# Kernel tuning notes

Measured on AMD Instinct MI355X. Metric: run time of the kernel, lower is better.

## Reference

```python
import jax, jax.numpy as jnp
import numpy as np

B, T, D, H = 512, 128, 256, 512  # batch, seq_len, input_dim, hidden_dim
L = T  # dense output size == seq_len


def setup_inputs() -> dict:
    key = jax.random.key(0)
    ks = jax.random.split(key, 12)
    s = 0.05
    return {
        "inputs": jax.random.normal(ks[0], (B, T, D), jnp.float32),
        "target_indices": jax.random.randint(ks[1], (B, T), 0, T),
        "enc_Wih": jax.random.normal(ks[2], (4 * H, D), jnp.float32) * s,
        "enc_Whh": jax.random.normal(ks[3], (4 * H, H), jnp.float32) * s,
        "enc_bih": jnp.zeros((4 * H,), jnp.float32),
        "enc_bhh": jnp.zeros((4 * H,), jnp.float32),
        "dec_Wih": jax.random.normal(ks[4], (4 * H, D), jnp.float32) * s,
        "dec_Whh": jax.random.normal(ks[5], (4 * H, H), jnp.float32) * s,
        "dec_bih": jnp.zeros((4 * H,), jnp.float32),
        "dec_bhh": jnp.zeros((4 * H,), jnp.float32),
        "Wd": jax.random.normal(ks[6], (L, H), jnp.float32) * s,
        "bd": jnp.zeros((L,), jnp.float32),
        "Wr": jax.random.normal(ks[7], (4, H), jnp.float32) * (2.0 / np.sqrt(H)),
        "br": jnp.zeros((4,), jnp.float32),
    }


def _lstm_cell(x, h, c, Wih, Whh, bih, bhh):
    gates = x @ Wih.T + h @ Whh.T + bih + bhh
    i, f, g, o = jnp.split(gates, 4, axis=-1)  # torch gate order i,f,g,o
    c = jax.nn.sigmoid(f) * c + jax.nn.sigmoid(i) * jnp.tanh(g)
    h = jax.nn.sigmoid(o) * jnp.tanh(c)
    return h, c


def reference(inputs, target_indices, enc_Wih, enc_Whh, enc_bih, enc_bhh,
              dec_Wih, dec_Whh, dec_bih, dec_bhh, Wd, bd, Wr, br):
    b, t, d = inputs.shape
    hdim = enc_Whh.shape[1]

    # Encoder LSTM over time (identical every step in the original -> compute once)
    def enc_step(carry, x_t):
        h, c = carry
        h, c = _lstm_cell(x_t, h, c, enc_Wih, enc_Whh, enc_bih, enc_bhh)
        return (h, c), h

    h0 = jnp.zeros((b, hdim), inputs.dtype)
    _, enc_hs = jax.lax.scan(enc_step, (h0, h0), inputs.transpose(1, 0, 2))
    enc = enc_hs.transpose(1, 0, 2)  # [B, T, H]

    batch_ar = jnp.arange(b)

    def dec_step(carry, idx_t):
        h, c, mask, x = carry
        h, c = _lstm_cell(x, h, c, dec_Wih, dec_Whh, dec_bih, dec_bhh)
        scores = jnp.einsum('bh,bth->bt', h, enc)
        attn = jax.nn.softmax(scores, axis=-1)
        ctx = jnp.einsum('bt,bth->bh', attn, enc)
        logits = ctx @ Wd.T + bd                       # [B, L]
        logits = jnp.where(mask > 0, -jnp.inf, logits)  # mask previously selected
        rot = ctx @ Wr.T + br                          # [B, 4]
        idx = jnp.clip(idx_t, 0, t - 1)
        mask = jnp.maximum(mask, jax.nn.one_hot(idx, mask.shape[1], dtype=mask.dtype))
        x_next = inputs[batch_ar, idx]
        return (h, c, mask, x_next), (logits, rot)

    mask0 = jnp.zeros((b, Wd.shape[0]), inputs.dtype)
    x0 = jnp.zeros((b, d), inputs.dtype)
    _, (all_logits, all_rot) = jax.lax.scan(
        dec_step, (h0, h0, mask0, x0), target_indices.T)
    return all_logits.transpose(1, 0, 2), all_rot.transpose(1, 0, 2)
```

## Files before the change

kernel.cpp:

```cpp
#include <hip/hip_runtime.h>
#include <hip/hip_bf16.h>
#include <hip/hip_fp16.h>
#include <math.h>

#define B_ 512
#define T_ 128
#define D_ 256
#define H_ 512
#define L_ 128

#define NEG_BIG (-1e30f)

typedef __hip_bfloat16 bf16;
typedef _Float16 f16x8 __attribute__((ext_vector_type(8)));
typedef float f32x4 __attribute__((ext_vector_type(4)));

__device__ __forceinline__ f32x4 mfma16(f16x8 a, f16x8 b, f32x4 c) {
  return __builtin_amdgcn_mfma_f32_16x16x32_f16(a, b, c, 0, 0, 0);
}

__device__ __forceinline__ float sigm(float x) { return 1.0f / (1.0f + expf(-x)); }

__device__ __forceinline__ float bf2f_bits(unsigned short u) {
  unsigned int i = ((unsigned int)u) << 16;
  float f; __builtin_memcpy(&f, &i, 4);
  return f;
}
__device__ __forceinline__ unsigned short f2bf_bits(float f) {
  unsigned int i; __builtin_memcpy(&i, &f, 4);
  unsigned int r = i + 0x7FFFu + ((i >> 16) & 1u);
  return (unsigned short)(r >> 16);
}

template <int F32>
__device__ __forceinline__ float ld1t(const void* base, size_t idx) {
  if (F32) return ((const float*)base)[idx];
  unsigned short u; __builtin_memcpy(&u, (const bf16*)base + idx, 2);
  return bf2f_bits(u);
}
template <int F32>
__device__ __forceinline__ void load8t(const void* base, size_t idx, float* d) {
  if (F32) {
    float4 x = *(const float4*)((const float*)base + idx);
    float4 y = *(const float4*)((const float*)base + idx + 4);
    d[0] = x.x; d[1] = x.y; d[2] = x.z; d[3] = x.w;
    d[4] = y.x; d[5] = y.y; d[6] = y.z; d[7] = y.w;
  } else {
    union { float4 f4; unsigned short u[8]; } q;
    q.f4 = *(const float4*)((const bf16*)base + idx);
#pragma unroll
    for (int i = 0; i < 8; ++i) d[i] = bf2f_bits(q.u[i]);
  }
}
template <int F32>
__device__ __forceinline__ void st1t(void* base, size_t idx, float v) {
  if (F32) ((float*)base)[idx] = v;
  else {
    unsigned short u = f2bf_bits(v);
    __builtin_memcpy((bf16*)base + idx, &u, 2);
  }
}

__global__ void probe_kernel(const void* x, int* flag) {
  __shared__ int cnt;
  if (threadIdx.x == 0) cnt = 0;
  __syncthreads();
  const unsigned short* u = (const unsigned short*)x;
  int wild = 0;
  for (int i = threadIdx.x; i < 16384; i += 256) {
    float v = bf2f_bits(u[2 * i]);
    float av = fabsf(v);
    if (!(av <= 1024.0f) || (v != 0.0f && av < 1e-20f)) wild++;
  }
  atomicAdd(&cnt, wild);
  __syncthreads();
  if (threadIdx.x == 0) flag[0] = (cnt > 512) ? 1 : 0;
}

__global__ void zero_kernel(float* __restrict__ p, int n4) {
  int i = blockIdx.x * blockDim.x + threadIdx.x;
  if (i < n4) ((float4*)p)[i] = make_float4(0.f, 0.f, 0.f, 0.f);
}

__global__ void first_sel_kernel(const int* __restrict__ tidx, int* __restrict__ fs) {
  __shared__ int row[L_];
  __shared__ int idxs[T_];
  int b = blockIdx.x;
  row[threadIdx.x] = 1 << 30;
  int v = tidx[b * T_ + threadIdx.x];
  idxs[threadIdx.x] = min(max(v, 0), T_ - 1);
  __syncthreads();
  if (threadIdx.x == 0) {
    for (int s = 0; s < T_; ++s) {
      int idx = idxs[s];
      if (row[idx] > s) row[idx] = s;
    }
  }
  __syncthreads();
  fs[b * L_ + threadIdx.x] = row[threadIdx.x];
}

template <int F32>
__device__ void pack_w_body(const void* Wih, const void* Whh, const void* bih,
                            const void* bhh, __half* Wpk, float* bs) {
  int np = blockIdx.x;
  int g = np & 3, j = np >> 2;
  int worig = g * H_ + j;
  for (int k = threadIdx.x; k < D_ + H_; k += 256) {
    float v = (k < D_) ? ld1t<F32>(Wih, (size_t)worig * D_ + k)
                       : ld1t<F32>(Whh, (size_t)worig * H_ + (k - D_));
    Wpk[(size_t)np * (D_ + H_) + k] = __float2half(v);
  }
  if (threadIdx.x == 0)
    bs[np] = ld1t<F32>(bih, worig) + ld1t<F32>(bhh, worig);
}
__global__ __launch_bounds__(256) void pack_w(const void* Wih, const void* Whh,
    const void* bih, const void* bhh, __half* Wpk, float* bs, const int* flagp) {
  if (*flagp) pack_w_body<1>(Wih, Whh, bih, bhh, Wpk, bs);
  else        pack_w_body<0>(Wih, Whh, bih, bhh, Wpk, bs);
}

template <int F32>
__device__ void pack16_body(const void* src, __half* dst, int n8) {
  int i = blockIdx.x * blockDim.x + threadIdx.x;
  if (i >= n8) return;
  float w[8];
  load8t<F32>(src, (size_t)i * 8, w);
  union { float4 f4; __half h[8]; } u;
#pragma unroll
  for (int q = 0; q < 8; ++q) u.h[q] = __float2half(w[q]);
  *(float4*)(dst + (size_t)i * 8) = u.f4;
}
__global__ __launch_bounds__(256) void pack16(const void* src, __half* dst, int n8,
                                              const int* flagp) {
  if (*flagp) pack16_body<1>(src, dst, n8);
  else        pack16_body<0>(src, dst, n8);
}

__global__ __launch_bounds__(256) void gather_x(const __half* __restrict__ X16,
                                                const int* __restrict__ tidx,
                                                __half* __restrict__ Xdec) {
  const int row = blockIdx.x * 8 + (threadIdx.x >> 5);
  const int c8 = (threadIdx.x & 31) * 8;
  const int b = row >> 7;
  const int s = row & (T_ - 1);
  float4 v;
  if (s == 0) {
    v = make_float4(0.f, 0.f, 0.f, 0.f);
  } else {
    int tsel = min(max(tidx[b * T_ + s - 1], 0), T_ - 1);
    v = *(const float4*)(X16 + ((size_t)b * T_ + tsel) * D_ + c8);
  }
  *(float4*)(Xdec + (size_t)row * D_ + c8) = v;
}

__global__ __launch_bounds__(256) void transpose_enc(const __half* __restrict__ enc,
                                                     __half* __restrict__ encT) {
  __shared__ __half tile[32][33];
  const int b = blockIdx.x;
  const int t0 = blockIdx.y * 32;
  const int h0 = blockIdx.z * 32;
  const int c = threadIdx.x & 31;
  const int r = threadIdx.x >> 5;
#pragma unroll
  for (int rr = 0; rr < 32; rr += 8)
    tile[rr + r][c] = enc[((size_t)b * T_ + t0 + rr + r) * H_ + h0 + c];
  __syncthreads();
#pragma unroll
  for (int rr = 0; rr < 32; rr += 8)
    encT[((size_t)b * H_ + h0 + rr + r) * T_ + t0 + c] = tile[c][rr + r];
}

#define SWZ(b, j) ((j) ^ (((b) & 7) << 2))

__device__ __forceinline__ void cell_f(const f32x4& acc, const float4& bias,
                                       float& c, float* hh) {
  float gi = acc[0] + bias.x;
  float gf = acc[1] + bias.y;
  float gg = acc[2] + bias.z;
  float go = acc[3] + bias.w;
  c = sigm(gf) * c + sigm(gi) * tanhf(gg);
  *hh = sigm(go) * tanhf(c);
}

template <int FAST>
__device__ void lstm_chain(const __half* __restrict__ Xp,
                           const __half* __restrict__ Wpk,
                           const float* __restrict__ bs,
                           __half* __restrict__ hbuf,
                           int tile, int bg, int* __restrict__ flags) {
  __shared__ __half hstage[32][32];
  const int tid = threadIdx.x;
  const int lane = tid & 63;
  const int w = tid >> 6;
  const int r15 = lane & 15;
  const int g4 = lane >> 4;
  const int m0 = tile * 128 + w * 32;
  const int b0 = bg * 32;
  const int bb0 = b0 + r15;
  const int bb1 = bb0 + 16;
  const int fl = lane & 15;
  const f32x4 z4 = {0.f, 0.f, 0.f, 0.f};

  const __half* aXp0 = Wpk + (size_t)(m0 + r15) * (D_ + H_) + g4 * 8;
  const __half* aXp1 = aXp0 + (size_t)16 * (D_ + H_);
  f16x8 aH0[16], aH1[16];
#pragma unroll
  for (int ks = 0; ks < 16; ++ks) {
    aH0[ks] = *(const f16x8*)(aXp0 + D_ + ks * 32);
    aH1[ks] = *(const f16x8*)(aXp1 + D_ + ks * 32);
  }
  const int nb0 = m0 + g4 * 4;
  const float4 bias0 = *(const float4*)(bs + nb0);
  const float4 bias1 = *(const float4*)(bs + nb0 + 16);
  const int jrel0 = w * 8 + g4;
  const int jrel1 = jrel0 + 4;
  float c00 = 0.f, c01 = 0.f, c10 = 0.f, c11 = 0.f;
  const int srow = tid >> 3;
  const int schk = tid & 7;
  const int sposl = SWZ(srow, schk * 4);
  unsigned long long* gdst = (unsigned long long*)hbuf;
  const size_t gcol = (size_t)tile * 32 + schk * 4;

  for (int t = 0; t < T_; ++t) {
    f32x4 acc00 = z4, acc01 = z4, acc10 = z4, acc11 = z4;
    {
      const __half* x0p = Xp + ((size_t)bb0 * T_ + t) * D_ + g4 * 8;
      const __half* x1p = Xp + ((size_t)bb1 * T_ + t) * D_ + g4 * 8;
#pragma unroll
      for (int ks = 0; ks < 8; ++ks) {
        f16x8 a0 = *(const f16x8*)(aXp0 + ks * 32);
        f16x8 a1 = *(const f16x8*)(aXp1 + ks * 32);
        f16x8 bx0 = *(const f16x8*)(x0p + ks * 32);
        f16x8 bx1 = *(const f16x8*)(x1p + ks * 32);
        acc00 = mfma16(a0, bx0, acc00);
        acc01 = mfma16(a0, bx1, acc01);
        acc10 = mfma16(a1, bx0, acc10);
        acc11 = mfma16(a1, bx1, acc11);
      }
    }
    if (t) {
      int v = __hip_atomic_load(flags + fl, __ATOMIC_RELAXED,
                                __HIP_MEMORY_SCOPE_AGENT);
      while (!__all(v >= t)) {
        __builtin_amdgcn_s_sleep(1);
        v = __hip_atomic_load(flags + fl, __ATOMIC_RELAXED,
                              __HIP_MEMORY_SCOPE_AGENT);
      }
      const __half* h0p = hbuf + ((size_t)bb0 * T_ + (t - 1)) * H_ + g4 * 8;
      const __half* h1p = hbuf + ((size_t)bb1 * T_ + (t - 1)) * H_ + g4 * 8;
      asm volatile("" : "+v"(h0p), "+v"(h1p));
#pragma unroll
      for (int ks = 0; ks < 16; ++ks) {
        f16x8 bh0 = *(const f16x8*)(h0p + ks * 32);
        f16x8 bh1 = *(const f16x8*)(h1p + ks * 32);
        acc00 = mfma16(aH0[ks], bh0, acc00);
        acc01 = mfma16(aH0[ks], bh1, acc01);
        acc10 = mfma16(aH1[ks], bh0, acc10);
        acc11 = mfma16(aH1[ks], bh1, acc11);
      }
    }
    float h00, h01, h10, h11;
    cell_f(acc00, bias0, c00, &h00);
    cell_f(acc01, bias0, c01, &h01);
    cell_f(acc10, bias1, c10, &h10);
    cell_f(acc11, bias1, c11, &h11);
    hstage[r15][SWZ(r15, jrel0)] = __float2half(h00);
    hstage[r15 + 16][SWZ(r15 + 16, jrel0)] = __float2half(h01);
    hstage[r15][SWZ(r15, jrel1)] = __float2half(h10);
    hstage[r15 + 16][SWZ(r15 + 16, jrel1)] = __float2half(h11);
    __syncthreads();
    {
      unsigned long long val =
          *(const unsigned long long*)&hstage[srow][sposl];
      size_t gi = ((((size_t)(b0 + srow) * T_ + t) * H_) + gcol) >> 2;
      if (FAST)
        gdst[gi] = val;
      else
        __hip_atomic_store(gdst + gi, val, __ATOMIC_RELAXED,
                           __HIP_MEMORY_SCOPE_AGENT);
    }
    if (t + 1 < T_) {
      __syncthreads();
      if (tid == 0)
        __hip_atomic_store(flags + tile, t + 1, __ATOMIC_RELAXED,
                           __HIP_MEMORY_SCOPE_AGENT);
    }
  }
}

__global__ __launch_bounds__(256, 2) void lstm_persist(
    const __half* __restrict__ Xenc, const __half* __restrict__ Xdec,
    const __half* __restrict__ WpkE, const float* __restrict__ bsE,
    const __half* __restrict__ WpkD, const float* __restrict__ bsD,
    __half* __restrict__ enc, __half* __restrict__ hdec, int* __restrict__ bar) {
  const int wgid = blockIdx.x;
  const int xcd = wgid & 7;
  const int tile = (wgid >> 3) & 15;
  const int q = wgid >> 7;
  const int g = q * 8 + xcd;
  const int p = g >> 4;
  const int bg = g & 15;
  int* flags = bar + g * 16;
  int* xcca = bar + 512 + g * 16;
  const int tid = threadIdx.x;
  const int lane = tid & 63;

  int xcc;
  asm volatile("s_getreg_b32 %0, hwreg(HW_REG_XCC_ID)" : "=s"(xcc));
  if (tid == 0)
    __hip_atomic_store(xcca + tile, xcc + 1, __ATOMIC_RELAXED,
                       __HIP_MEMORY_SCOPE_AGENT);
  int vv = __hip_atomic_load(xcca + (lane & 15), __ATOMIC_RELAXED,
                             __HIP_MEMORY_SCOPE_AGENT);
  while (!__all(vv != 0)) {
    __builtin_amdgcn_s_sleep(1);
    vv = __hip_atomic_load(xcca + (lane & 15), __ATOMIC_RELAXED,
                           __HIP_MEMORY_SCOPE_AGENT);
  }
  const int fast = __all(vv == (xcc + 1));

  if (p == 0) {
    if (fast) lstm_chain<1>(Xenc, WpkE, bsE, enc, tile, bg, flags);
    else      lstm_chain<0>(Xenc, WpkE, bsE, enc, tile, bg, flags);
  } else {
    if (fast) lstm_chain<1>(Xdec, WpkD, bsD, hdec, tile, bg, flags);
    else      lstm_chain<0>(Xdec, WpkD, bsD, hdec, tile, bg, flags);
  }
}

template <int F32>
__device__ void attend_body(const __half* __restrict__ hdec, const __half* __restrict__ enc,
                            const __half* __restrict__ encT, const __half* __restrict__ Wd16,
                            const void* __restrict__ bd, const void* __restrict__ Wr,
                            const void* __restrict__ br, const int* __restrict__ fs,
                            void* __restrict__ out) {
  __shared__ __align__(16) __half Plds[4][16 * 128];
  __shared__ __align__(16) __half Clds[4][16 * 128];
  const int b = blockIdx.x;
  const int sbase = blockIdx.y * 64;
  const int tid = threadIdx.x;
  const int lane = tid & 63;
  const int w = tid >> 6;
  const int r15 = lane & 15;
  const int g4 = lane >> 4;
  const int sw = sbase + w * 16;
  const __half* encb = enc + (size_t)b * T_ * H_;
  const f32x4 z4 = {0.f, 0.f, 0.f, 0.f};
  f32x4 sacc[8];
#pragma unroll
  for (int i = 0; i < 8; ++i) sacc[i] = z4;
  {
    const __half* hdp = hdec + ((size_t)b * T_ + (sw + r15)) * H_ + g4 * 8;
    for (int k0 = 0; k0 < H_; k0 += 32) {
      f16x8 bv = *(const f16x8*)(hdp + k0);
      const __half* ap = encb + (size_t)r15 * H_ + g4 * 8 + k0;
#pragma unroll
      for (int ms = 0; ms < 8; ++ms)
        sacc[ms] = mfma16(*(const f16x8*)(ap + (size_t)ms * 16 * H_), bv, sacc[ms]);
    }
  }
  float mx = -INFINITY;
#pragma unroll
  for (int ms = 0; ms < 8; ++ms)
#pragma unroll
    for (int q = 0; q < 4; ++q) mx = fmaxf(mx, sacc[ms][q]);
  mx = fmaxf(mx, __shfl_xor(mx, 16));
  mx = fmaxf(mx, __shfl_xor(mx, 32));
  float sum = 0.f;
  float pv[32];
#pragma unroll
  for (int ms = 0; ms < 8; ++ms)
#pragma unroll
    for (int q = 0; q < 4; ++q) {
      float e = expf(sacc[ms][q] - mx);
      pv[ms * 4 + q] = e;
      sum += e;
    }
  sum += __shfl_xor(sum, 16);
  sum += __shfl_xor(sum, 32);
  const float inv = 1.0f / sum;
  {
    char* pw = (char*)Plds[w];
    const int swz = (r15 & 7) << 4;
#pragma unroll
    for (int ms = 0; ms < 8; ++ms)
#pragma unroll
      for (int q = 0; q < 4; ++q) {
        int t = ms * 16 + g4 * 4 + q;
        *(__half*)(pw + r15 * 256 + ((t * 2) ^ swz)) = __float2half(pv[ms * 4 + q] * inv);
      }
  }
  __syncthreads();
  f32x4 lacc[8];
#pragma unroll
  for (int i = 0; i < 8; ++i) lacc[i] = z4;
  float racc = 0.f;
  const int sl4 = lane >> 2;
  const int rr4 = lane & 3;
  const char* pr = (const char*)Plds[w];
  char* cw = (char*)Clds[w];
  const char* cr = (const char*)Clds[w];
  const int aswz = (r15 & 7) << 4;
  for (int hc = 0; hc < 4; ++hc) {
    f32x4 cacc[8];
#pragma unroll
    for (int i = 0; i < 8; ++i) cacc[i] = z4;
#pragma unroll
    for (int k0 = 0; k0 < T_; k0 += 32) {
      f16x8 av = *(const f16x8*)(pr + r15 * 256 + (((k0 + g4 * 8) * 2) ^ aswz));
      const __half* bp = encT + ((size_t)b * H_ + hc * 128 + r15) * T_ + g4 * 8 + k0;
#pragma unroll
      for (int ns = 0; ns < 8; ++ns)
        cacc[ns] = mfma16(av, *(const f16x8*)(bp + (size_t)ns * 16 * T_), cacc[ns]);
    }
    __syncthreads();
#pragma unroll
    for (int ns = 0; ns < 8; ++ns)
#pragma unroll
      for (int q = 0; q < 4; ++q) {
        int s = g4 * 4 + q;
        int h2 = (ns * 16 + r15) * 2;
        *(__half*)(cw + s * 256 + (h2 ^ ((s & 7) << 4))) = __float2half(cacc[ns][q]);
      }
    __syncthreads();
#pragma unroll
    for (int kk = 0; kk < 128; kk += 32) {
      f16x8 av = *(const f16x8*)(cr + r15 * 256 + (((kk + g4 * 8) * 2) ^ aswz));
      const __half* wp = Wd16 + (size_t)r15 * H_ + hc * 128 + kk + g4 * 8;
#pragma unroll
      for (int nl = 0; nl < 8; ++nl)
        lacc[nl] = mfma16(av, *(const f16x8*)(wp + (size_t)nl * 16 * H_), lacc[nl]);
    }
    {
      const int rswz = (sl4 & 7) << 4;
#pragma unroll
      for (int g = 0; g < 16; ++g) {
        union { float4 f4; __half h[8]; } u;
        u.f4 = *(const float4*)(cr + sl4 * 256 + ((g * 16) ^ rswz));
#pragma unroll
        for (int q = 0; q < 8; ++q)
          racc += __half2float(u.h[q]) *
                  ld1t<F32>(Wr, (size_t)rr4 * H_ + hc * 128 + g * 8 + q);
      }
    }
  }
#pragma unroll
  for (int nl = 0; nl < 8; ++nl)
#pragma unroll
    for (int q = 0; q < 4; ++q) {
      int sg = sw + g4 * 4 + q;
      int l = nl * 16 + r15;
      float v = lacc[nl][q] + ld1t<F32>(bd, l);
      if (fs[b * L_ + l] < sg) v = NEG_BIG;
      st1t<F32>(out, ((size_t)b * T_ + sg) * L_ + l, v);
    }
  {
    float v = racc + ld1t<F32>(br, rr4);
    st1t<F32>(out, (size_t)B_ * T_ * L_ + ((size_t)b * T_ + (sw + sl4)) * 4 + rr4, v);
  }
}

__global__ __launch_bounds__(256) void attend_mfma(
    const __half* hdec, const __half* enc, const __half* encT, const __half* Wd16,
    const void* bd, const void* Wr, const void* br, const int* fs, void* out,
    const int* flagp) {
  if (*flagp) attend_body<1>(hdec, enc, encT, Wd16, bd, Wr, br, fs, out);
  else        attend_body<0>(hdec, enc, encT, Wd16, bd, Wr, br, fs, out);
}

static inline size_t al256(size_t x) { return (x + 255) & ~(size_t)255; }

extern "C" void kernel_launch(void* const* d_in, const int* in_sizes, int n_in,
                              void* d_out, int out_size, void* d_ws, size_t ws_size,
                              hipStream_t stream) {
  const void* inputs = d_in[0];
  const int* tidx = (const int*)d_in[1];
  const void* eWih = d_in[2];
  const void* eWhh = d_in[3];
  const void* eBih = d_in[4];
  const void* eBhh = d_in[5];
  const void* dWih = d_in[6];
  const void* dWhh = d_in[7];
  const void* dBih = d_in[8];
  const void* dBhh = d_in[9];
  const void* Wd = d_in[10];
  const void* bd = d_in[11];
  const void* Wr = d_in[12];
  const void* br = d_in[13];

  char* pp = (char*)d_ws;
  int* flag = (int*)pp;        pp += 256;
  int* fs = (int*)pp;          pp += al256((size_t)B_ * L_ * 4);
  __half* WpkE = (__half*)pp;  pp += (size_t)4 * H_ * (D_ + H_) * 2;
  __half* WpkD = (__half*)pp;  pp += (size_t)4 * H_ * (D_ + H_) * 2;
  float* bsE = (float*)pp;     pp += (size_t)4 * H_ * 4;
  float* bsD = (float*)pp;     pp += (size_t)4 * H_ * 4;
  __half* Wd16 = (__half*)pp;  pp += (size_t)L_ * H_ * 2;
  __half* X16 = (__half*)pp;   pp += (size_t)B_ * T_ * D_ * 2;
  __half* enc = (__half*)pp;   pp += (size_t)B_ * T_ * H_ * 2;
  __half* encT = (__half*)pp;  pp += (size_t)B_ * H_ * T_ * 2;
  __half* hdec = (__half*)pp;  pp += (size_t)B_ * T_ * H_ * 2;
  int* bar = (int*)pp;         pp += 8192;
  __half* Xdec = encT;

  probe_kernel<<<1, 256, 0, stream>>>(inputs, flag);
  pack_w<<<4 * H_, 256, 0, stream>>>(eWih, eWhh, eBih, eBhh, WpkE, bsE, flag);
  pack_w<<<4 * H_, 256, 0, stream>>>(dWih, dWhh, dBih, dBhh, WpkD, bsD, flag);
  pack16<<<(B_ * T_ * D_ / 8 + 255) / 256, 256, 0, stream>>>(
      inputs, X16, B_ * T_ * D_ / 8, flag);
  pack16<<<(L_ * H_ / 8 + 255) / 256, 256, 0, stream>>>(Wd, Wd16, L_ * H_ / 8, flag);
  first_sel_kernel<<<B_, 128, 0, stream>>>(tidx, fs);
  gather_x<<<B_ * T_ / 8, 256, 0, stream>>>(X16, tidx, Xdec);
  zero_kernel<<<2, 256, 0, stream>>>((float*)bar, 512);

  lstm_persist<<<512, 256, 0, stream>>>(X16, Xdec, WpkE, bsE, WpkD, bsD,
                                        enc, hdec, bar);

  transpose_enc<<<dim3(B_, T_ / 32, H_ / 32), 256, 0, stream>>>(enc, encT);

  attend_mfma<<<dim3(B_, 2), 256, 0, stream>>>(hdec, enc, encT, Wd16, bd, Wr, br,
                                               fs, d_out, flag);
}
```

Before: 2.347 ms.

## Stage input-weight fragments in LDS, pin one in registers, use fast exp activations

```diff
diff --git a/kernel.cpp b/kernel.cpp
--- a/kernel.cpp
+++ b/kernel.cpp
@@ -19,7 +19,10 @@
   return __builtin_amdgcn_mfma_f32_16x16x32_f16(a, b, c, 0, 0, 0);
 }
 
-__device__ __forceinline__ float sigm(float x) { return 1.0f / (1.0f + expf(-x)); }
+__device__ __forceinline__ float fsigm(float x) { return 1.0f / (1.0f + __expf(-x)); }
+__device__ __forceinline__ float ftanh(float x) {
+  return 1.0f - 2.0f / (__expf(2.0f * x) + 1.0f);
+}
 
 __device__ __forceinline__ float bf2f_bits(unsigned short u) {
   unsigned int i = ((unsigned int)u) << 16;
@@ -179,8 +182,8 @@
   float gf = acc[1] + bias.y;
   float gg = acc[2] + bias.z;
   float go = acc[3] + bias.w;
-  c = sigm(gf) * c + sigm(gi) * tanhf(gg);
-  *hh = sigm(go) * tanhf(c);
+  c = fsigm(gf) * c + fsigm(gi) * ftanh(gg);
+  *hh = fsigm(go) * ftanh(c);
 }
 
 template <int FAST>
@@ -189,6 +192,7 @@
                            const float* __restrict__ bs,
                            __half* __restrict__ hbuf,
                            int tile, int bg, int* __restrict__ flags) {
+  __shared__ __half Wx[56 * 512];
   __shared__ __half hstage[32][32];
   const int tid = threadIdx.x;
   const int lane = tid & 63;
@@ -204,12 +208,27 @@
 
   const __half* aXp0 = Wpk + (size_t)(m0 + r15) * (D_ + H_) + g4 * 8;
   const __half* aXp1 = aXp0 + (size_t)16 * (D_ + H_);
+
+  __half* wl0 = &Wx[(size_t)(w * 14 + 0) * 512 + lane * 8];
+  __half* wl1 = &Wx[(size_t)(w * 14 + 7) * 512 + lane * 8];
+#pragma unroll
+  for (int ks = 0; ks < 7; ++ks) {
+    *(f16x8*)(wl0 + ks * 512) = *(const f16x8*)(aXp0 + ks * 32);
+    *(f16x8*)(wl1 + ks * 512) = *(const f16x8*)(aXp1 + ks * 32);
+  }
   f16x8 aH0[16], aH1[16];
 #pragma unroll
   for (int ks = 0; ks < 16; ++ks) {
     aH0[ks] = *(const f16x8*)(aXp0 + D_ + ks * 32);
     aH1[ks] = *(const f16x8*)(aXp1 + D_ + ks * 32);
   }
+#pragma unroll
+  for (int ks = 0; ks < 16; ++ks)
+    asm("" : "+v"(aH0[ks]), "+v"(aH1[ks]));
+  f16x8 aX7_0 = *(const f16x8*)(aXp0 + 7 * 32);
+  f16x8 aX7_1 = *(const f16x8*)(aXp1 + 7 * 32);
+  asm("" : "+v"(aX7_0), "+v"(aX7_1));
+
   const int nb0 = m0 + g4 * 4;
   const float4 bias0 = *(const float4*)(bs + nb0);
   const float4 bias1 = *(const float4*)(bs + nb0 + 16);
@@ -221,16 +240,17 @@
   const int sposl = SWZ(srow, schk * 4);
   unsigned long long* gdst = (unsigned long long*)hbuf;
   const size_t gcol = (size_t)tile * 32 + schk * 4;
+  __syncthreads();
 
   for (int t = 0; t < T_; ++t) {
     f32x4 acc00 = z4, acc01 = z4, acc10 = z4, acc11 = z4;
     {
       const __half* x0p = Xp + ((size_t)bb0 * T_ + t) * D_ + g4 * 8;
       const __half* x1p = Xp + ((size_t)bb1 * T_ + t) * D_ + g4 * 8;
-#pragma unroll
-      for (int ks = 0; ks < 8; ++ks) {
-        f16x8 a0 = *(const f16x8*)(aXp0 + ks * 32);
-        f16x8 a1 = *(const f16x8*)(aXp1 + ks * 32);
+#pragma unroll 4
+      for (int ks = 0; ks < 7; ++ks) {
+        f16x8 a0 = *(const f16x8*)(wl0 + ks * 512);
+        f16x8 a1 = *(const f16x8*)(wl1 + ks * 512);
         f16x8 bx0 = *(const f16x8*)(x0p + ks * 32);
         f16x8 bx1 = *(const f16x8*)(x1p + ks * 32);
         acc00 = mfma16(a0, bx0, acc00);
@@ -238,6 +258,12 @@
         acc10 = mfma16(a1, bx0, acc10);
         acc11 = mfma16(a1, bx1, acc11);
       }
+      f16x8 bx0 = *(const f16x8*)(x0p + 7 * 32);
+      f16x8 bx1 = *(const f16x8*)(x1p + 7 * 32);
+      acc00 = mfma16(aX7_0, bx0, acc00);
+      acc01 = mfma16(aX7_0, bx1, acc01);
+      acc10 = mfma16(aX7_1, bx0, acc10);
+      acc11 = mfma16(aX7_1, bx1, acc11);
     }
     if (t) {
       int v = __hip_atomic_load(flags + fl, __ATOMIC_RELAXED,
@@ -250,7 +276,7 @@
       const __half* h0p = hbuf + ((size_t)bb0 * T_ + (t - 1)) * H_ + g4 * 8;
       const __half* h1p = hbuf + ((size_t)bb1 * T_ + (t - 1)) * H_ + g4 * 8;
       asm volatile("" : "+v"(h0p), "+v"(h1p));
-#pragma unroll
+#pragma unroll 4
       for (int ks = 0; ks < 16; ++ks) {
         f16x8 bh0 = *(const f16x8*)(h0p + ks * 32);
         f16x8 bh1 = *(const f16x8*)(h1p + ks * 32);
```

Result: slower. 4.130 ms (+75.9%).
